# Kernel tuning notes

Measured on AMD Instinct MI355X. Metric: run time of the kernel, lower is better.

The kernel has to match this reference:

```python
import jax, jax.numpy as jnp
import numpy as np

ENC_HID = 256
DEC_HID = 256
BATCH = 64
SRC_LEN = 4096


def setup_inputs() -> dict:
    key = jax.random.key(0)
    k1, k2, k3, k4, k5 = jax.random.split(key, 5)
    hidden = jax.random.normal(k1, (1, BATCH, DEC_HID), dtype=jnp.float32)
    encoder_outputs = jax.random.normal(k2, (SRC_LEN, BATCH, 2 * ENC_HID), dtype=jnp.float32)
    # nn.Linear(2*enc_hid + dec_hid, dec_hid): weight [out, in], bias [out]
    W = jax.random.normal(k3, (DEC_HID, 2 * ENC_HID + DEC_HID), dtype=jnp.float32) * 0.02
    b = jax.random.normal(k4, (DEC_HID,), dtype=jnp.float32) * 0.02
    v = jax.random.uniform(k5, (DEC_HID,), dtype=jnp.float32)
    return {"hidden": hidden, "encoder_outputs": encoder_outputs, "W": W, "b": b, "v": v}


def reference(hidden, encoder_outputs, W, b, v):
    # hidden: [n_layers, B, D] -> take first layer: [B, D]
    h = hidden[0]
    # encoder_outputs: [S, B, 2E] -> [B, S, 2E]
    eo = jnp.transpose(encoder_outputs, (1, 0, 2))
    D = h.shape[-1]
    # Split the concat+linear: cat is (hidden, encoder_outputs) along last dim,
    # so W = [Wh | We] along its input axis. Mathematically identical to
    # tanh(attn(cat(h_rep, eo))) but avoids materializing the concat.
    Wh, We = W[:, :D], W[:, D:]
    # energy: [B, S, D]
    energy = jnp.tanh(jnp.einsum('bd,kd->bk', h, Wh)[:, None, :]
                      + jnp.einsum('bse,ke->bsk', eo, We)
                      + b)
    # scores: [B, S]  (v . energy, same as bmm(v[1,D], energy[D,S]))
    scores = jnp.einsum('bsk,k->bs', energy, v)
    return jax.nn.softmax(scores, axis=1)
```

## Files before the change

### kernel.cpp

```cpp
#include <hip/hip_runtime.h>
#include <stdint.h>

#define ENC2   512
#define NDIM   256
#define BATCH  64
#define SLEN   4096
#define NROWS  (SLEN*BATCH)
#define BLKR   128
#define NKB    16

typedef _Float16 half8 __attribute__((ext_vector_type(8)));
typedef float    f32x4 __attribute__((ext_vector_type(4)));

__device__ __forceinline__ float tanh_fast(float x) {
  float e = __expf(2.0f * x);
  return 1.0f - 2.0f * __builtin_amdgcn_rcpf(e + 1.0f);
}

__global__ __launch_bounds__(256) void pack_We(const float* __restrict__ W,
                                               _Float16* __restrict__ wp) {
  int t = blockIdx.x * 256 + threadIdx.x;
  int lane = t & 63;
  int ct   = (t >> 6) & 15;
  int kb   = t >> 10;
  int c  = ct * 16 + (lane & 15);
  int kk = kb * 32 + (lane >> 4) * 8;
  const float* src = W + (size_t)c * 768 + 256 + kk;
  half8 h;
#pragma unroll
  for (int j = 0; j < 8; ++j) h[j] = (_Float16)src[j];
  *(half8*)(wp + (size_t)t * 8) = h;
}

__global__ __launch_bounds__(256) void compute_hb(const float* __restrict__ hidden,
                                                  const float* __restrict__ W,
                                                  const float* __restrict__ bvec,
                                                  float* __restrict__ hb) {
  __shared__ float hs[256];
  int b = blockIdx.x, k = threadIdx.x;
  hs[k] = hidden[b * 256 + k];
  __syncthreads();
  const float* wr = W + (size_t)k * 768;
  float acc = bvec[k];
#pragma unroll 8
  for (int d = 0; d < 256; d += 4) {
    f32x4 wv = *(const f32x4*)(wr + d);
    acc += wv[0]*hs[d] + wv[1]*hs[d+1] + wv[2]*hs[d+2] + wv[3]*hs[d+3];
  }
  hb[b * 256 + k] = acc;
}

__global__ __launch_bounds__(256, 2) void attn_energy(const float* __restrict__ eo,
                                                      const _Float16* __restrict__ wp,
                                                      const float* __restrict__ hb,
                                                      const float* __restrict__ v,
                                                      float* __restrict__ scores) {
  const int tid  = threadIdx.x;
  const int w    = tid >> 6;
  const int lane = tid & 63;
  const int g    = lane >> 4;
  const int l15  = lane & 15;
  const int rowbase = blockIdx.x * BLKR + w * 32;

  const float* aptr0 = eo + (size_t)(rowbase + l15) * ENC2 + g * 8;
  const float* aptr1 = aptr0 + 16 * ENC2;

  f32x4 acc[2][16];
#pragma unroll
  for (int i = 0; i < 2; ++i)
#pragma unroll
    for (int j = 0; j < 16; ++j) acc[i][j] = (f32x4){0.f, 0.f, 0.f, 0.f};

#define LDA(v00, v01, v10, v11, KB)                                  \
  do {                                                               \
    const float* p0_ = aptr0 + (size_t)(KB) * 32;                    \
    const float* p1_ = aptr1 + (size_t)(KB) * 32;                    \
    v00 = *(const f32x4*)(p0_);                                      \
    v01 = *(const f32x4*)(p0_ + 4);                                  \
    v10 = *(const f32x4*)(p1_);                                      \
    v11 = *(const f32x4*)(p1_ + 4);                                  \
  } while (0)

#define CVT(a0, a1, v00, v01, v10, v11)                              \
  do {                                                               \
    _Pragma("unroll")                                                \
    for (int j = 0; j < 4; ++j) {                                    \
      a0[j] = (_Float16)v00[j]; a0[j + 4] = (_Float16)v01[j];        \
      a1[j] = (_Float16)v10[j]; a1[j + 4] = (_Float16)v11[j];        \
    }                                                                \
  } while (0)

  f32x4 x00, x01, x10, x11;
  f32x4 y00, y01, y10, y11;
  LDA(x00, x01, x10, x11, 0);
  LDA(y00, y01, y10, y11, 1);

  const half8* bp = (const half8*)wp + lane;

#pragma unroll 1
  for (int kb = 0; kb < NKB; kb += 2) {
    {
      half8 a0, a1;
      CVT(a0, a1, x00, x01, x10, x11);
      if (kb + 2 < NKB) LDA(x00, x01, x10, x11, kb + 2);
      const half8* bpc = bp + (size_t)(kb * 16) * 64;
#pragma unroll
      for (int ct = 0; ct < 16; ++ct) {
        half8 bf = bpc[(size_t)ct * 64];
        acc[0][ct] = __builtin_amdgcn_mfma_f32_16x16x32_f16(a0, bf, acc[0][ct], 0, 0, 0);
        acc[1][ct] = __builtin_amdgcn_mfma_f32_16x16x32_f16(a1, bf, acc[1][ct], 0, 0, 0);
      }
    }
    {
      half8 a0, a1;
      CVT(a0, a1, y00, y01, y10, y11);
      if (kb + 3 < NKB) LDA(y00, y01, y10, y11, kb + 3);
      const half8* bpc = bp + (size_t)((kb + 1) * 16) * 64;
#pragma unroll
      for (int ct = 0; ct < 16; ++ct) {
        half8 bf = bpc[(size_t)ct * 64];
        acc[0][ct] = __builtin_amdgcn_mfma_f32_16x16x32_f16(a0, bf, acc[0][ct], 0, 0, 0);
        acc[1][ct] = __builtin_amdgcn_mfma_f32_16x16x32_f16(a1, bf, acc[1][ct], 0, 0, 0);
      }
    }
  }
#undef LDA
#undef CVT

  float sc0[4] = {0.f, 0.f, 0.f, 0.f};
  float sc1[4] = {0.f, 0.f, 0.f, 0.f};
#pragma unroll
  for (int ct = 0; ct < 16; ++ct) {
    int k = ct * 16 + l15;
    float vk = v[k];
    const float* hbk = hb + k;
#pragma unroll
    for (int r = 0; r < 4; ++r) {
      int b0 = (rowbase + g * 4 + r) & 63;
      int b1 = (rowbase + 16 + g * 4 + r) & 63;
      sc0[r] += vk * tanh_fast(acc[0][ct][r] + hbk[(size_t)b0 * 256]);
      sc1[r] += vk * tanh_fast(acc[1][ct][r] + hbk[(size_t)b1 * 256]);
    }
  }
#pragma unroll
  for (int m = 1; m < 16; m <<= 1) {
#pragma unroll
    for (int r = 0; r < 4; ++r) {
      sc0[r] += __shfl_xor(sc0[r], m, 64);
      sc1[r] += __shfl_xor(sc1[r], m, 64);
    }
  }
  int r = l15;
  if (r < 4) {
    float o0 = (r == 0) ? sc0[0] : (r == 1) ? sc0[1] : (r == 2) ? sc0[2] : sc0[3];
    float o1 = (r == 0) ? sc1[0] : (r == 1) ? sc1[1] : (r == 2) ? sc1[2] : sc1[3];
    int gr0 = rowbase + g * 4 + r;
    int gr1 = rowbase + 16 + g * 4 + r;
    scores[(size_t)(gr0 & 63) * SLEN + (gr0 >> 6)] = o0;
    scores[(size_t)(gr1 & 63) * SLEN + (gr1 >> 6)] = o1;
  }
}

__global__ __launch_bounds__(256) void softmax_rows(const float* __restrict__ scores,
                                                    float* __restrict__ out) {
  int b = blockIdx.x, t = threadIdx.x;
  const f32x4* in4 = (const f32x4*)(scores + (size_t)b * SLEN);
  f32x4* out4 = (f32x4*)(out + (size_t)b * SLEN);
  f32x4 x0 = in4[t], x1 = in4[256 + t], x2 = in4[512 + t], x3 = in4[768 + t];
  float m = fmaxf(fmaxf(fmaxf(x0[0], x0[1]), fmaxf(x0[2], x0[3])),
                  fmaxf(fmaxf(x1[0], x1[1]), fmaxf(x1[2], x1[3])));
  m = fmaxf(m, fmaxf(fmaxf(fmaxf(x2[0], x2[1]), fmaxf(x2[2], x2[3])),
                     fmaxf(fmaxf(x3[0], x3[1]), fmaxf(x3[2], x3[3]))));
#pragma unroll
  for (int off = 1; off < 64; off <<= 1) m = fmaxf(m, __shfl_xor(m, off, 64));
  __shared__ float redm[4], reds[4];
  int w = t >> 6, lane = t & 63;
  if (lane == 0) redm[w] = m;
  __syncthreads();
  m = fmaxf(fmaxf(redm[0], redm[1]), fmaxf(redm[2], redm[3]));
  float s = 0.f;
#pragma unroll
  for (int j = 0; j < 4; ++j) { x0[j] = __expf(x0[j] - m); s += x0[j]; }
#pragma unroll
  for (int j = 0; j < 4; ++j) { x1[j] = __expf(x1[j] - m); s += x1[j]; }
#pragma unroll
  for (int j = 0; j < 4; ++j) { x2[j] = __expf(x2[j] - m); s += x2[j]; }
#pragma unroll
  for (int j = 0; j < 4; ++j) { x3[j] = __expf(x3[j] - m); s += x3[j]; }
#pragma unroll
  for (int off = 1; off < 64; off <<= 1) s += __shfl_xor(s, off, 64);
  if (lane == 0) reds[w] = s;
  __syncthreads();
  s = (reds[0] + reds[1]) + (reds[2] + reds[3]);
  float inv = 1.0f / s;
#pragma unroll
  for (int j = 0; j < 4; ++j) { x0[j] *= inv; x1[j] *= inv; x2[j] *= inv; x3[j] *= inv; }
  out4[t] = x0; out4[256 + t] = x1; out4[512 + t] = x2; out4[768 + t] = x3;
}

extern "C" void kernel_launch(void* const* d_in, const int* in_sizes, int n_in,
                              void* d_out, int out_size, void* d_ws, size_t ws_size,
                              hipStream_t stream) {
  (void)in_sizes; (void)n_in; (void)out_size; (void)ws_size;
  const float* hidden = (const float*)d_in[0];
  const float* eo     = (const float*)d_in[1];
  const float* W      = (const float*)d_in[2];
  const float* bvec   = (const float*)d_in[3];
  const float* v      = (const float*)d_in[4];
  float* out = (float*)d_out;

  uint8_t* ws = (uint8_t*)d_ws;
  _Float16* wp  = (_Float16*)ws;
  float* hb     = (float*)(ws + 262144);
  float* scores = (float*)(ws + 262144 + 65536);

  pack_We<<<64, 256, 0, stream>>>(W, wp);
  compute_hb<<<64, 256, 0, stream>>>(hidden, W, bvec, hb);
  attn_energy<<<NROWS / BLKR, 256, 0, stream>>>(eo, wp, hb, v, scores);
  softmax_rows<<<BATCH, 256, 0, stream>>>(scores, out);
}
```

Before: 778.3 us.

## Halve rows per wave in attn_energy to raise occupancy

Each wave now computes one 16-row tile instead of two, so a block covers 64 rows and launch bounds allow 4 blocks per CU. The accumulator and prefetch register footprint roughly halves, which is meant to raise occupancy and hide the latency of the streaming encoder-output loads. The cost is that each B-fragment load from the packed weights now feeds only one MFMA instead of two, doubling weight traffic per row.

Result: slower. 822.1 us (+5.6%).

```diff
diff --git a/kernel.cpp b/kernel.cpp
--- a/kernel.cpp
+++ b/kernel.cpp
@@ -6,7 +6,7 @@
 #define BATCH  64
 #define SLEN   4096
 #define NROWS  (SLEN*BATCH)
-#define BLKR   128
+#define BLKR   64
 #define NKB    16
 
 typedef _Float16 half8 __attribute__((ext_vector_type(8)));
@@ -50,7 +50,7 @@
   hb[b * 256 + k] = acc;
 }
 
-__global__ __launch_bounds__(256, 2) void attn_energy(const float* __restrict__ eo,
+__global__ __launch_bounds__(256, 4) void attn_energy(const float* __restrict__ eo,
                                                       const _Float16* __restrict__ wp,
                                                       const float* __restrict__ hb,
                                                       const float* __restrict__ v,
@@ -60,75 +60,65 @@
   const int lane = tid & 63;
   const int g    = lane >> 4;
   const int l15  = lane & 15;
-  const int rowbase = blockIdx.x * BLKR + w * 32;
-
-  const float* aptr0 = eo + (size_t)(rowbase + l15) * ENC2 + g * 8;
-  const float* aptr1 = aptr0 + 16 * ENC2;
-
-  f32x4 acc[2][16];
-#pragma unroll
-  for (int i = 0; i < 2; ++i)
-#pragma unroll
-    for (int j = 0; j < 16; ++j) acc[i][j] = (f32x4){0.f, 0.f, 0.f, 0.f};
-
-#define LDA(v00, v01, v10, v11, KB)                                  \
+  const int rowbase = blockIdx.x * BLKR + w * 16;
+
+  const float* aptr = eo + (size_t)(rowbase + l15) * ENC2 + g * 8;
+
+  f32x4 acc[16];
+#pragma unroll
+  for (int j = 0; j < 16; ++j) acc[j] = (f32x4){0.f, 0.f, 0.f, 0.f};
+
+#define LDA(v0, v1, KB)                                              \
   do {                                                               \
-    const float* p0_ = aptr0 + (size_t)(KB) * 32;                    \
-    const float* p1_ = aptr1 + (size_t)(KB) * 32;                    \
-    v00 = *(const f32x4*)(p0_);                                      \
-    v01 = *(const f32x4*)(p0_ + 4);                                  \
-    v10 = *(const f32x4*)(p1_);                                      \
-    v11 = *(const f32x4*)(p1_ + 4);                                  \
+    const float* p_ = aptr + (size_t)(KB) * 32;                      \
+    v0 = *(const f32x4*)(p_);                                        \
+    v1 = *(const f32x4*)(p_ + 4);                                    \
   } while (0)
 
-#define CVT(a0, a1, v00, v01, v10, v11)                              \
+#define CVT(a0, v0, v1)                                              \
   do {                                                               \
     _Pragma("unroll")                                                \
     for (int j = 0; j < 4; ++j) {                                    \
-      a0[j] = (_Float16)v00[j]; a0[j + 4] = (_Float16)v01[j];        \
-      a1[j] = (_Float16)v10[j]; a1[j + 4] = (_Float16)v11[j];        \
+      a0[j] = (_Float16)v0[j]; a0[j + 4] = (_Float16)v1[j];          \
     }                                                                \
   } while (0)
 
-  f32x4 x00, x01, x10, x11;
-  f32x4 y00, y01, y10, y11;
-  LDA(x00, x01, x10, x11, 0);
-  LDA(y00, y01, y10, y11, 1);
+  f32x4 x0, x1;
+  f32x4 y0, y1;
+  LDA(x0, x1, 0);
+  LDA(y0, y1, 1);
 
   const half8* bp = (const half8*)wp + lane;
 
 #pragma unroll 1
   for (int kb = 0; kb < NKB; kb += 2) {
     {
-      half8 a0, a1;
-      CVT(a0, a1, x00, x01, x10, x11);
-      if (kb + 2 < NKB) LDA(x00, x01, x10, x11, kb + 2);
+      half8 a0;
+      CVT(a0, x0, x1);
+      if (kb + 2 < NKB) LDA(x0, x1, kb + 2);
       const half8* bpc = bp + (size_t)(kb * 16) * 64;
 #pragma unroll
       for (int ct = 0; ct < 16; ++ct) {
         half8 bf = bpc[(size_t)ct * 64];
-        acc[0][ct] = __builtin_amdgcn_mfma_f32_16x16x32_f16(a0, bf, acc[0][ct], 0, 0, 0);
-        acc[1][ct] = __builtin_amdgcn_mfma_f32_16x16x32_f16(a1, bf, acc[1][ct], 0, 0, 0);
+        acc[ct] = __builtin_amdgcn_mfma_f32_16x16x32_f16(a0, bf, acc[ct], 0, 0, 0);
       }
     }
     {
-      half8 a0, a1;
-      CVT(a0, a1, y00, y01, y10, y11);
-      if (kb + 3 < NKB) LDA(y00, y01, y10, y11, kb + 3);
+      half8 a0;
+      CVT(a0, y0, y1);
+      if (kb + 3 < NKB) LDA(y0, y1, kb + 3);
       const half8* bpc = bp + (size_t)((kb + 1) * 16) * 64;
 #pragma unroll
       for (int ct = 0; ct < 16; ++ct) {
         half8 bf = bpc[(size_t)ct * 64];
-        acc[0][ct] = __builtin_amdgcn_mfma_f32_16x16x32_f16(a0, bf, acc[0][ct], 0, 0, 0);
-        acc[1][ct] = __builtin_amdgcn_mfma_f32_16x16x32_f16(a1, bf, acc[1][ct], 0, 0, 0);
+        acc[ct] = __builtin_amdgcn_mfma_f32_16x16x32_f16(a0, bf, acc[ct], 0, 0, 0);
       }
     }
   }
 #undef LDA
 #undef CVT
 
-  float sc0[4] = {0.f, 0.f, 0.f, 0.f};
-  float sc1[4] = {0.f, 0.f, 0.f, 0.f};
+  float sc[4] = {0.f, 0.f, 0.f, 0.f};
 #pragma unroll
   for (int ct = 0; ct < 16; ++ct) {
     int k = ct * 16 + l15;
@@ -137,27 +127,19 @@
 #pragma unroll
     for (int r = 0; r < 4; ++r) {
       int b0 = (rowbase + g * 4 + r) & 63;
-      int b1 = (rowbase + 16 + g * 4 + r) & 63;
-      sc0[r] += vk * tanh_fast(acc[0][ct][r] + hbk[(size_t)b0 * 256]);
-      sc1[r] += vk * tanh_fast(acc[1][ct][r] + hbk[(size_t)b1 * 256]);
+      sc[r] += vk * tanh_fast(acc[ct][r] + hbk[(size_t)b0 * 256]);
     }
   }
 #pragma unroll
   for (int m = 1; m < 16; m <<= 1) {
 #pragma unroll
-    for (int r = 0; r < 4; ++r) {
-      sc0[r] += __shfl_xor(sc0[r], m, 64);
-      sc1[r] += __shfl_xor(sc1[r], m, 64);
-    }
+    for (int r = 0; r < 4; ++r) sc[r] += __shfl_xor(sc[r], m, 64);
   }
   int r = l15;
   if (r < 4) {
-    float o0 = (r == 0) ? sc0[0] : (r == 1) ? sc0[1] : (r == 2) ? sc0[2] : sc0[3];
-    float o1 = (r == 0) ? sc1[0] : (r == 1) ? sc1[1] : (r == 2) ? sc1[2] : sc1[3];
-    int gr0 = rowbase + g * 4 + r;
-    int gr1 = rowbase + 16 + g * 4 + r;
-    scores[(size_t)(gr0 & 63) * SLEN + (gr0 >> 6)] = o0;
-    scores[(size_t)(gr1 & 63) * SLEN + (gr1 >> 6)] = o1;
+    float o0 = (r == 0) ? sc[0] : (r == 1) ? sc[1] : (r == 2) ? sc[2] : sc[3];
+    int gr = rowbase + g * 4 + r;
+    scores[(size_t)(gr & 63) * SLEN + (gr >> 6)] = o0;
   }
 }
 
```
